# Kernel optimization log

Hardware: AMD Instinct MI355X
Metric: run time of the kernel (lower is better)

## Reference

```python
import jax, jax.numpy as jnp
import numpy as np

B, N, C, H, F = 4, 256, 256, 8, 64  # batch, nodes, in_channels, heads, n_hidden


def setup_inputs() -> dict:
    key = jax.random.key(0)
    k1, k2, k3, k4, k5 = jax.random.split(key, 5)
    x = jax.random.normal(k1, (B, N, C), jnp.float32)
    W_l = jax.random.normal(k2, (C, H * F), jnp.float32) / np.sqrt(C)
    W_r = jax.random.normal(k3, (C, H * F), jnp.float32) / np.sqrt(C)
    attn_w = jax.random.normal(k4, (F,), jnp.float32) / np.sqrt(F)
    adj = jax.random.randint(k5, (N, N, H), 0, 2, jnp.int32)
    # guarantee at least one unmasked head per (i, j) pair so the
    # softmax-over-heads (dim=-1 in the source) never sees all -inf
    adj = adj.at[:, :, 0].set(1)
    return {"x": x, "W_l": W_l, "W_r": W_r, "attn_w": attn_w, "adj": adj}


def reference(x, W_l, W_r, attn_w, adj):
    b, n, _ = x.shape
    g_l = (x @ W_l).reshape(b, n, H, F)
    g_r = (x @ W_r).reshape(b, n, H, F)
    # torch: g_l.repeat(1,n,1,1) + g_r.repeat_interleave(n,dim=1), then
    # view(b,n,n,h,f)  =>  g_sum[b,i,j,h,f] = g_r[b,i] + g_l[b,j]
    g_sum = g_r[:, :, None] + g_l[:, None, :]          # [b,i,j,h,f]
    e = jnp.einsum('bijhf,f->bijh', jax.nn.leaky_relu(g_sum, 0.2), attn_w)
    e = jnp.where(adj == 0, -jnp.inf, e)               # adj broadcasts over batch
    a = jax.nn.softmax(e, axis=-1)                     # softmax over heads, per source (dim=-1)
    out = jnp.einsum('bijh,bjhf->bihf', a, g_r)        # aggregate over neighbors j
    return out.reshape(b, n, H * F)                    # is_concat=True
```

## Files before the change

kernel.cpp:

```cpp
#include <hip/hip_runtime.h>
#include <hip/hip_bf16.h>

typedef _Float16 h2 __attribute__((ext_vector_type(2)));

constexpr int kB = 4, kN = 256, kC = 256, kH = 8, kF = 64, kHF = 512;
constexpr int kIPB = 4;

union H2U { h2 h; unsigned int u; };

__global__ __launch_bounds__(256) void gat_gemm_kernel(
    const float* __restrict__ x,
    const float* __restrict__ Wl,
    const float* __restrict__ Wr,
    unsigned int* __restrict__ gl,
    unsigned int* __restrict__ gr)
{
    __shared__ float xs[4][kC];
    const int rowBase = blockIdx.x * 4;
    const float* Wm = (blockIdx.y == 0) ? Wl : Wr;
    unsigned int* gout = (blockIdx.y == 0) ? gl : gr;

    const int tid = threadIdx.x;

    {
        const int r = tid >> 6;
        const int kc = (tid & 63) * 4;
        *(float4*)&xs[r][kc] = *(const float4*)(x + (rowBase + r) * kC + kc);
    }
    __syncthreads();

    const int c0 = tid * 2;
    float acc[4][2];
#pragma unroll
    for (int r = 0; r < 4; ++r) { acc[r][0] = 0.f; acc[r][1] = 0.f; }

    for (int k = 0; k < kC; k += 4) {
        float2 wv[4];
#pragma unroll
        for (int kk = 0; kk < 4; ++kk)
            wv[kk] = *(const float2*)(Wm + (k + kk) * kHF + c0);
#pragma unroll
        for (int r = 0; r < 4; ++r) {
            float4 xv = *(const float4*)&xs[r][k];
            acc[r][0] = fmaf(xv.x, wv[0].x, acc[r][0]);
            acc[r][1] = fmaf(xv.x, wv[0].y, acc[r][1]);
            acc[r][0] = fmaf(xv.y, wv[1].x, acc[r][0]);
            acc[r][1] = fmaf(xv.y, wv[1].y, acc[r][1]);
            acc[r][0] = fmaf(xv.z, wv[2].x, acc[r][0]);
            acc[r][1] = fmaf(xv.z, wv[2].y, acc[r][1]);
            acc[r][0] = fmaf(xv.w, wv[3].x, acc[r][0]);
            acc[r][1] = fmaf(xv.w, wv[3].y, acc[r][1]);
        }
    }

#pragma unroll
    for (int r = 0; r < 4; ++r) {
        H2U p; p.h = (h2){(_Float16)acc[r][0], (_Float16)acc[r][1]};
        gout[((rowBase + r) * kHF + c0) >> 1] = p.u;
    }
}

__global__ __launch_bounds__(1024, 4) void gat_attn_kernel(
    const unsigned int* __restrict__ gl,
    const unsigned int* __restrict__ gr,
    const float* __restrict__ attn_w,
    const int* __restrict__ adj,
    float* __restrict__ out)
{
    __shared__ float red[8 * kIPB * kHF];

    const int bi0 = blockIdx.x * kIPB;
    const int b = bi0 >> 8;
    const int i0 = bi0 & 255;
    const int tid = threadIdx.x;
    const int wv = tid >> 6;
    const int lane = tid & 63;
    const int h = lane >> 3;
    const int fg = lane & 7;
    const int fbase = fg * 8;

    h2 gri[kIPB][4];
#pragma unroll
    for (int ii = 0; ii < kIPB; ++ii) {
        uint4 pk = *(const uint4*)(gr +
            (((size_t)(bi0 + ii) * kHF + h * kF + fbase) >> 1));
        H2U a0, a1, a2, a3;
        a0.u = pk.x; a1.u = pk.y; a2.u = pk.z; a3.u = pk.w;
        gri[ii][0] = a0.h; gri[ii][1] = a1.h; gri[ii][2] = a2.h; gri[ii][3] = a3.h;
    }
    h2 w2[4];
    {
        float4 wa = *(const float4*)(attn_w + fbase);
        float4 wb = *(const float4*)(attn_w + fbase + 4);
        w2[0] = (h2){(_Float16)wa.x, (_Float16)wa.y};
        w2[1] = (h2){(_Float16)wa.z, (_Float16)wa.w};
        w2[2] = (h2){(_Float16)wb.x, (_Float16)wb.y};
        w2[3] = (h2){(_Float16)wb.z, (_Float16)wb.w};
    }

    float acc[kIPB][8];
#pragma unroll
    for (int ii = 0; ii < kIPB; ++ii)
#pragma unroll
        for (int q = 0; q < 8; ++q) acc[ii][q] = 0.f;

    const h2 c02 = (h2){(_Float16)0.2f, (_Float16)0.2f};
    const size_t gcolbase = (size_t)(b * kN) * kHF + h * kF + fbase;
    const int adjbase = i0 * kN * kH + h;

    size_t off = (gcolbase + (size_t)wv * kHF) >> 1;
    uint4 ga = *(const uint4*)(gl + off);
    uint4 gb = *(const uint4*)(gr + off);

    for (int j = wv; j < kN; j += 16) {
        const size_t offn = (gcolbase + (size_t)(j + 16) * kHF) >> 1;
        uint4 ga_n = *(const uint4*)(gl + offn);
        uint4 gb_n = *(const uint4*)(gr + offn);

        int am[kIPB];
#pragma unroll
        for (int ii = 0; ii < kIPB; ++ii)
            am[ii] = adj[adjbase + (ii * kN + j) * kH];

        h2 gl2[4], gr2[4];
        { H2U t; t.u = ga.x; gl2[0] = t.h; t.u = ga.y; gl2[1] = t.h;
                 t.u = ga.z; gl2[2] = t.h; t.u = ga.w; gl2[3] = t.h;
                 t.u = gb.x; gr2[0] = t.h; t.u = gb.y; gr2[1] = t.h;
                 t.u = gb.z; gr2[2] = t.h; t.u = gb.w; gr2[3] = t.h; }

        float grf[8];
#pragma unroll
        for (int q = 0; q < 4; ++q) {
            grf[2 * q]     = (float)gr2[q].x;
            grf[2 * q + 1] = (float)gr2[q].y;
        }

#pragma unroll
        for (int ii = 0; ii < kIPB; ++ii) {
            float e = 0.f;
#pragma unroll
            for (int q = 0; q < 4; ++q) {
                h2 s = gri[ii][q] + gl2[q];
                h2 u = __builtin_elementwise_max(s, c02 * s);
                e = __builtin_amdgcn_fdot2(u, w2[q], e, false);
            }
            e += __shfl_xor(e, 1);
            e += __shfl_xor(e, 2);
            e += __shfl_xor(e, 4);

            e = am[ii] ? e : -1e30f;

            float ex = __expf(e);
            float den = ex;
            den += __shfl_xor(den, 8);
            den += __shfl_xor(den, 16);
            den += __shfl_xor(den, 32);
            float a = ex * __builtin_amdgcn_rcpf(den);

#pragma unroll
            for (int q = 0; q < 8; ++q)
                acc[ii][q] = fmaf(a, grf[q], acc[ii][q]);
        }

        ga = ga_n; gb = gb_n;
    }

    if (wv >= 8) {
#pragma unroll
        for (int ii = 0; ii < kIPB; ++ii) {
            float* rp = &red[((wv - 8) * kIPB + ii) * kHF + lane * 8];
#pragma unroll
            for (int q = 0; q < 8; ++q) rp[q] = acc[ii][q];
        }
    }
    __syncthreads();
    if (wv < 8) {
#pragma unroll
        for (int ii = 0; ii < kIPB; ++ii) {
            float* rp = &red[(wv * kIPB + ii) * kHF + lane * 8];
#pragma unroll
            for (int q = 0; q < 8; ++q) rp[q] += acc[ii][q];
        }
    }
    __syncthreads();

#pragma unroll
    for (int t = tid; t < kIPB * kHF; t += 1024) {
        const int ii = t >> 9;
        const int c  = t & 511;
        float s = 0.f;
#pragma unroll
        for (int w8 = 0; w8 < 8; ++w8)
            s += red[(w8 * kIPB + ii) * kHF + c];
        out[(size_t)(bi0 + ii) * kHF + c] = s;
    }
}

extern "C" void kernel_launch(void* const* d_in, const int* in_sizes, int n_in,
                              void* d_out, int out_size, void* d_ws, size_t ws_size,
                              hipStream_t stream) {
    const float* x  = (const float*)d_in[0];
    const float* Wl = (const float*)d_in[1];
    const float* Wr = (const float*)d_in[2];
    const float* aw = (const float*)d_in[3];
    const int* adj  = (const int*)d_in[4];

    unsigned int* gl = (unsigned int*)d_ws;
    unsigned int* gr = gl + (size_t)kB * kN * kHF / 2;

    dim3 g1(kB * kN / 4, 2);
    gat_gemm_kernel<<<g1, 256, 0, stream>>>(x, Wl, Wr, gl, gr);

    gat_attn_kernel<<<kB * kN / kIPB, 1024, 0, stream>>>(
        gl, gr, aw, adj, (float*)d_out);
}
```

Measured before the change: 107.1 us.

## Split neighbor loop across two blocks, bitpack adjacency in LDS, accumulate in fp16

The attention kernel now splits the neighbor dimension j into two halves on a second grid axis, doubling the block count, and combines the partial results with atomicAdd into an output the GEMM kernel zero-fills. Adjacency for each block is preloaded with vector loads and packed into per-(i,j) byte masks in shared memory, replacing strided scalar global loads inside the loop. Aggregation accumulators move from fp32 to packed fp16 FMAs, and launch bounds change to request higher occupancy. The GEMM loop also software-prefetches the next W tile. The risks are fp16 accumulation error, atomic contention, and dropping the cross-iteration prefetch of g_l/g_r in the attention loop.

Result: slower. 112.7 us (+5.2%).

```diff
diff --git a/kernel.cpp b/kernel.cpp
--- a/kernel.cpp
+++ b/kernel.cpp
@@ -5,6 +5,7 @@
 
 constexpr int kB = 4, kN = 256, kC = 256, kH = 8, kF = 64, kHF = 512;
 constexpr int kIPB = 4;
+constexpr int kJS = 2;
 
 union H2U { h2 h; unsigned int u; };
 
@@ -13,7 +14,8 @@
     const float* __restrict__ Wl,
     const float* __restrict__ Wr,
     unsigned int* __restrict__ gl,
-    unsigned int* __restrict__ gr)
+    unsigned int* __restrict__ gr,
+    float* __restrict__ out)
 {
     __shared__ float xs[4][kC];
     const int rowBase = blockIdx.x * 4;
@@ -22,6 +24,12 @@
 
     const int tid = threadIdx.x;
 
+    if (blockIdx.y == 0) {
+        float4 z = make_float4(0.f, 0.f, 0.f, 0.f);
+        float4* o = (float4*)out + blockIdx.x * 512 + tid * 2;
+        o[0] = z; o[1] = z;
+    }
+
     {
         const int r = tid >> 6;
         const int kc = (tid & 63) * 4;
@@ -34,11 +42,17 @@
 #pragma unroll
     for (int r = 0; r < 4; ++r) { acc[r][0] = 0.f; acc[r][1] = 0.f; }
 
+    float2 wv[4], wn[4];
+#pragma unroll
+    for (int kk = 0; kk < 4; ++kk)
+        wv[kk] = *(const float2*)(Wm + kk * kHF + c0);
+
     for (int k = 0; k < kC; k += 4) {
-        float2 wv[4];
-#pragma unroll
-        for (int kk = 0; kk < 4; ++kk)
-            wv[kk] = *(const float2*)(Wm + (k + kk) * kHF + c0);
+        if (k + 4 < kC) {
+#pragma unroll
+            for (int kk = 0; kk < 4; ++kk)
+                wn[kk] = *(const float2*)(Wm + (k + 4 + kk) * kHF + c0);
+        }
 #pragma unroll
         for (int r = 0; r < 4; ++r) {
             float4 xv = *(const float4*)&xs[r][k];
@@ -51,6 +65,8 @@
             acc[r][0] = fmaf(xv.w, wv[3].x, acc[r][0]);
             acc[r][1] = fmaf(xv.w, wv[3].y, acc[r][1]);
         }
+#pragma unroll
+        for (int kk = 0; kk < 4; ++kk) wv[kk] = wn[kk];
     }
 
 #pragma unroll
@@ -60,7 +76,7 @@
     }
 }
 
-__global__ __launch_bounds__(1024, 4) void gat_attn_kernel(
+__global__ __launch_bounds__(1024, 8) void gat_attn_kernel(
     const unsigned int* __restrict__ gl,
     const unsigned int* __restrict__ gr,
     const float* __restrict__ attn_w,
@@ -68,72 +84,74 @@
     float* __restrict__ out)
 {
     __shared__ float red[8 * kIPB * kHF];
+    __shared__ unsigned int msk[kN / kJS];
 
     const int bi0 = blockIdx.x * kIPB;
-    const int b = bi0 >> 8;
     const int i0 = bi0 & 255;
+    const int j0 = blockIdx.y * (kN / kJS);
     const int tid = threadIdx.x;
     const int wv = tid >> 6;
     const int lane = tid & 63;
     const int h = lane >> 3;
     const int fg = lane & 7;
-    const int fbase = fg * 8;
+
+    if (tid < 512) {
+        const int jj = tid & 127;
+        const int ii = tid >> 7;
+        const int* ap = adj + (i0 + ii) * (kN * kH) + (j0 + jj) * kH;
+        uint4 a0 = *(const uint4*)ap;
+        uint4 a1 = *(const uint4*)(ap + 4);
+        unsigned int m = 0;
+        m |= (a0.x != 0) << 0; m |= (a0.y != 0) << 1;
+        m |= (a0.z != 0) << 2; m |= (a0.w != 0) << 3;
+        m |= (a1.x != 0) << 4; m |= (a1.y != 0) << 5;
+        m |= (a1.z != 0) << 6; m |= (a1.w != 0) << 7;
+        ((unsigned char*)msk)[jj * 4 + ii] = (unsigned char)m;
+    }
 
     h2 gri[kIPB][4];
 #pragma unroll
     for (int ii = 0; ii < kIPB; ++ii) {
-        uint4 pk = *(const uint4*)(gr +
-            (((size_t)(bi0 + ii) * kHF + h * kF + fbase) >> 1));
+        uint4 pk = *(const uint4*)(gr + ((bi0 + ii) * 256 + h * 32 + fg * 4));
         H2U a0, a1, a2, a3;
         a0.u = pk.x; a1.u = pk.y; a2.u = pk.z; a3.u = pk.w;
         gri[ii][0] = a0.h; gri[ii][1] = a1.h; gri[ii][2] = a2.h; gri[ii][3] = a3.h;
     }
     h2 w2[4];
     {
-        float4 wa = *(const float4*)(attn_w + fbase);
-        float4 wb = *(const float4*)(attn_w + fbase + 4);
+        float4 wa = *(const float4*)(attn_w + fg * 8);
+        float4 wb = *(const float4*)(attn_w + fg * 8 + 4);
         w2[0] = (h2){(_Float16)wa.x, (_Float16)wa.y};
         w2[1] = (h2){(_Float16)wa.z, (_Float16)wa.w};
         w2[2] = (h2){(_Float16)wb.x, (_Float16)wb.y};
         w2[3] = (h2){(_Float16)wb.z, (_Float16)wb.w};
     }
 
-    float acc[kIPB][8];
+    h2 acc[kIPB][4];
 #pragma unroll
     for (int ii = 0; ii < kIPB; ++ii)
 #pragma unroll
-        for (int q = 0; q < 8; ++q) acc[ii][q] = 0.f;
+        for (int q = 0; q < 4; ++q) acc[ii][q] = (h2){(_Float16)0.f, (_Float16)0.f};
 
     const h2 c02 = (h2){(_Float16)0.2f, (_Float16)0.2f};
-    const size_t gcolbase = (size_t)(b * kN) * kHF + h * kF + fbase;
-    const int adjbase = i0 * kN * kH + h;
-
-    size_t off = (gcolbase + (size_t)wv * kHF) >> 1;
-    uint4 ga = *(const uint4*)(gl + off);
-    uint4 gb = *(const uint4*)(gr + off);
-
-    for (int j = wv; j < kN; j += 16) {
-        const size_t offn = (gcolbase + (size_t)(j + 16) * kHF) >> 1;
-        uint4 ga_n = *(const uint4*)(gl + offn);
-        uint4 gb_n = *(const uint4*)(gr + offn);
-
-        int am[kIPB];
-#pragma unroll
-        for (int ii = 0; ii < kIPB; ++ii)
-            am[ii] = adj[adjbase + (ii * kN + j) * kH];
+
+    __syncthreads();
+
+    unsigned int goff = (unsigned int)((bi0 >> 8) * (kN * 256)
+                                       + (j0 + wv) * 256 + h * 32 + fg * 4);
+
+    for (int it = 0; it < kN / kJS / 16; ++it) {
+        const int jl = wv + it * 16;
+        uint4 ga = *(const uint4*)(gl + goff);
+        uint4 gb = *(const uint4*)(gr + goff);
+        goff += 16 * 256;
+        const unsigned int m = msk[jl];
 
         h2 gl2[4], gr2[4];
         { H2U t; t.u = ga.x; gl2[0] = t.h; t.u = ga.y; gl2[1] = t.h;
                  t.u = ga.z; gl2[2] = t.h; t.u = ga.w; gl2[3] = t.h;
                  t.u = gb.x; gr2[0] = t.h; t.u = gb.y; gr2[1] = t.h;
                  t.u = gb.z; gr2[2] = t.h; t.u = gb.w; gr2[3] = t.h; }
-
-        float grf[8];
-#pragma unroll
-        for (int q = 0; q < 4; ++q) {
-            grf[2 * q]     = (float)gr2[q].x;
-            grf[2 * q + 1] = (float)gr2[q].y;
-        }
 
 #pragma unroll
         for (int ii = 0; ii < kIPB; ++ii) {
@@ -148,7 +166,8 @@
             e += __shfl_xor(e, 2);
             e += __shfl_xor(e, 4);
 
-            e = am[ii] ? e : -1e30f;
+            const unsigned int bit = (m >> (ii * 8 + h)) & 1u;
+            e = bit ? e : -1e30f;
 
             float ex = __expf(e);
             float den = ex;
@@ -157,12 +176,11 @@
             den += __shfl_xor(den, 32);
             float a = ex * __builtin_amdgcn_rcpf(den);
 
-#pragma unroll
-            for (int q = 0; q < 8; ++q)
-                acc[ii][q] = fmaf(a, grf[q], acc[ii][q]);
-        }
-
-        ga = ga_n; gb = gb_n;
+            const h2 a2 = (h2){(_Float16)a, (_Float16)a};
+#pragma unroll
+            for (int q = 0; q < 4; ++q)
+                acc[ii][q] = __builtin_elementwise_fma(a2, gr2[q], acc[ii][q]);
+        }
     }
 
     if (wv >= 8) {
@@ -170,7 +188,10 @@
         for (int ii = 0; ii < kIPB; ++ii) {
             float* rp = &red[((wv - 8) * kIPB + ii) * kHF + lane * 8];
 #pragma unroll
-            for (int q = 0; q < 8; ++q) rp[q] = acc[ii][q];
+            for (int q = 0; q < 4; ++q) {
+                float2 f = make_float2((float)acc[ii][q].x, (float)acc[ii][q].y);
+                *(float2*)&rp[q * 2] = f;
+            }
         }
     }
     __syncthreads();
@@ -179,7 +200,12 @@
         for (int ii = 0; ii < kIPB; ++ii) {
             float* rp = &red[(wv * kIPB + ii) * kHF + lane * 8];
 #pragma unroll
-            for (int q = 0; q < 8; ++q) rp[q] += acc[ii][q];
+            for (int q = 0; q < 4; ++q) {
+                float2 f = *(float2*)&rp[q * 2];
+                f.x += (float)acc[ii][q].x;
+                f.y += (float)acc[ii][q].y;
+                *(float2*)&rp[q * 2] = f;
+            }
         }
     }
     __syncthreads();
@@ -192,7 +218,7 @@
 #pragma unroll
         for (int w8 = 0; w8 < 8; ++w8)
             s += red[(w8 * kIPB + ii) * kHF + c];
-        out[(size_t)(bi0 + ii) * kHF + c] = s;
+        atomicAdd(&out[(bi0 + ii) * kHF + c], s);
     }
 }
 
@@ -209,8 +235,9 @@
     unsigned int* gr = gl + (size_t)kB * kN * kHF / 2;
 
     dim3 g1(kB * kN / 4, 2);
-    gat_gemm_kernel<<<g1, 256, 0, stream>>>(x, Wl, Wr, gl, gr);
-
-    gat_attn_kernel<<<kB * kN / kIPB, 1024, 0, stream>>>(
+    gat_gemm_kernel<<<g1, 256, 0, stream>>>(x, Wl, Wr, gl, gr, (float*)d_out);
+
+    dim3 g2(kB * kN / kIPB, kJS);
+    gat_attn_kernel<<<g2, 1024, 0, stream>>>(
         gl, gr, aw, adj, (float*)d_out);
 }
```
